# Kernel tuning notes

Measured on AMD Instinct MI355X. Metric: run time of the kernel, lower is better.

The kernel has to match this reference:

```python
import jax, jax.numpy as jnp
import numpy as np

IMAGE_SIZE = 192
NEAR = 0.1
FAR = 100.0
EPS = 1e-3
BACKGROUND = (0.0, 0.0, 0.0)


def setup_inputs() -> dict:
    key = jax.random.key(0)
    k1, k2, k3, k4 = jax.random.split(key, 4)
    B, F, T = 2, 512, 4
    centers = jax.random.uniform(k1, (B, F, 1, 2), minval=-0.9, maxval=0.9)
    offsets = jax.random.normal(k2, (B, F, 3, 2)) * 0.08
    xy = centers + offsets  # triangle vertices in NDC [-1, 1]
    z = jax.random.uniform(k3, (B, F, 3, 1), minval=1.0, maxval=10.0)  # inside (near, far)
    faces = jnp.concatenate([xy, z], axis=-1).astype(jnp.float32)  # [B,F,3,3]
    textures = jax.random.uniform(k4, (B, F, T, T, T, 3), dtype=jnp.float32)
    return {"faces": faces, "textures": textures}


def _face_inv(v):
    # v: [..., 3 verts, 3 (x,y,z)]. Rows of cofactor matrix / det give barycentric coeffs
    # so that w_k = row_k . (px, py, 1), matching rasterize_cuda's face_inv.
    x0, y0 = v[..., 0, 0], v[..., 0, 1]
    x1, y1 = v[..., 1, 0], v[..., 1, 1]
    x2, y2 = v[..., 2, 0], v[..., 2, 1]
    det = x2 * (y0 - y1) + x0 * (y1 - y2) + x1 * (y2 - y0)
    det = jnp.where(jnp.abs(det) < 1e-12, 1e-12, det)
    rows = jnp.stack([
        y1 - y2, x2 - x1, x1 * y2 - x2 * y1,
        y2 - y0, x0 - x2, x2 * y0 - x0 * y2,
        y0 - y1, x1 - x0, x0 * y1 - x1 * y0], axis=-1)
    return rows.reshape(v.shape[:-2] + (3, 3)) / det[..., None, None]


def _rasterize(faces, textures):
    B, F = faces.shape[:2]
    T = textures.shape[2]
    IS = IMAGE_SIZE
    P = IS * IS
    # pixel centers in NDC, matching (2*i + 1 - is) / is in the CUDA kernel
    coord = (2.0 * jnp.arange(IS, dtype=faces.dtype) + 1.0 - IS) / IS
    yp, xp = jnp.meshgrid(coord, coord, indexing="ij")
    xp = xp.reshape(P)
    yp = yp.reshape(P)
    pc = jnp.stack([xp, yp, jnp.ones((P,), faces.dtype)], axis=-1)  # [P,3]

    x = faces[..., 0]
    y = faces[..., 1]
    z = faces[..., 2]  # [B,F,3]
    # backface culling (skip if (y2-y0)*(x1-x0) < (y1-y0)*(x2-x0))
    front = (y[..., 2] - y[..., 0]) * (x[..., 1] - x[..., 0]) >= \
            (x[..., 2] - x[..., 0]) * (y[..., 1] - y[..., 0])  # [B,F]

    def edge_ok(a, b):
        # pixel on inner side of edge a->b: (yp-ya)*(xb-xa) >= (xp-xa)*(yb-ya)
        return ((yp[None, None, :] - y[..., a:a + 1]) * (x[..., b:b + 1] - x[..., a:a + 1])
                >= (xp[None, None, :] - x[..., a:a + 1]) * (y[..., b:b + 1] - y[..., a:a + 1]))

    inside = edge_ok(0, 1) & edge_ok(1, 2) & edge_ok(2, 0)  # [B,F,P]

    finv = _face_inv(faces)  # [B,F,3,3]
    w = jnp.einsum("bfkc,pc->bfpk", finv, pc)  # barycentric weights [B,F,P,3]
    w = jnp.clip(w, 0.0, 1.0)
    w = w / jnp.maximum(jnp.sum(w, axis=-1, keepdims=True), 1e-12)
    # perspective-correct depth: 1/zp = sum_k w_k / z_k
    zp = 1.0 / jnp.maximum(jnp.einsum("bfpk,bfk->bfp", w, 1.0 / z), 1e-12)
    valid = front[..., None] & inside & (zp > NEAR) & (zp < FAR)
    depth_c = jnp.where(valid, zp, FAR)
    depth_map = jnp.min(depth_c, axis=1)  # z-buffer [B,P]
    fidx = jnp.argmin(depth_c, axis=1)    # winning face per pixel (ties -> lowest index)
    found = depth_map < FAR

    # gather barycentric weights / vertices of the winning face
    wwin = jnp.take_along_axis(w, fidx[:, None, :, None], axis=1)[:, 0]  # [B,P,3]
    vwin = jax.vmap(lambda f, i: f[i])(faces, fidx)  # [B,P,3,3]
    zwin = vwin[..., 2]  # [B,P,3]

    # texture-cube trilinear sampling with perspective-corrected weights
    tif = wwin * (T - 1) * (depth_map[..., None] / zwin)
    tif = jnp.clip(tif, 0.0, T - 1 - EPS)
    tlo_f = jnp.floor(tif)
    frac = tif - tlo_f
    tlo = tlo_f.astype(jnp.int32)
    bits = (jnp.arange(8)[:, None] >> jnp.arange(3)[None, :]) & 1  # [8,3] corner offsets
    idx = tlo[..., None, :] + bits  # [B,P,8,3], in [0, T-1]
    cw = jnp.prod(jnp.where(bits.astype(bool), frac[..., None, :], 1.0 - frac[..., None, :]), axis=-1)  # [B,P,8]
    fsafe = jnp.maximum(fidx, 0)
    flat = ((fsafe[..., None] * T + idx[..., 0]) * T + idx[..., 1]) * T + idx[..., 2]  # [B,P,8]
    texf = textures.reshape(B, F * T * T * T, 3)
    samp = jax.vmap(lambda t, i: t[i])(texf, flat)  # [B,P,8,3]
    rgb = jnp.sum(cw[..., None] * samp, axis=-2)  # [B,P,3]
    bg = jnp.asarray(BACKGROUND, dtype=rgb.dtype)
    rgb = jnp.where(found[..., None], rgb, bg)  # background compositing

    rgb_map = rgb.reshape(B, IS, IS, 3)
    alpha_map = found.astype(faces.dtype).reshape(B, 1, IS, IS)  # single part (part_mask=None)
    depth_out = depth_map.reshape(B, IS, IS)
    return rgb_map, alpha_map, depth_out


def reference(faces, textures):
    return _rasterize(faces, textures)
```

## Files before the change

kernel.cpp:

```cpp
#include <hip/hip_runtime.h>

#define IS     192
#define F_CNT  512
#define TEX    4
#define NEARF  0.1f
#define FARF   100.0f

struct FaceData {
    float xmin, xmax, ymin, ymax;
    float x0, y0, x1, y1, x2, y2;
    float f00, f01, f02, f10, f11, f12, f20, f21, f22;
    float iz0, iz1, iz2;
    float z0, z1, z2;
};

__global__ __launch_bounds__(256) void raster_kernel(
    const float* __restrict__ faces,
    const float* __restrict__ textures,
    float* __restrict__ out)
{
    __shared__ FaceData sf[F_CNT];
    __shared__ unsigned short sidx[F_CNT];
    __shared__ int scount;

    const int b   = blockIdx.z;
    const int tx0 = blockIdx.x * 16;
    const int ty0 = blockIdx.y * 16;
    const int tid = threadIdx.y * 16 + threadIdx.x;

    if (tid == 0) scount = 0;
    __syncthreads();

    const float xlo = (2.0f * tx0        + 1.0f - IS) / (float)IS;
    const float xhi = (2.0f * (tx0 + 15) + 1.0f - IS) / (float)IS;
    const float ylo = (2.0f * ty0        + 1.0f - IS) / (float)IS;
    const float yhi = (2.0f * (ty0 + 15) + 1.0f - IS) / (float)IS;

    for (int f = tid; f < F_CNT; f += 256) {
        const float* v = faces + ((size_t)b * F_CNT + f) * 9;
        const float x0 = v[0], y0 = v[1], z0 = v[2];
        const float x1 = v[3], y1 = v[4], z1 = v[5];
        const float x2 = v[6], y2 = v[7], z2 = v[8];

        const bool front = (y2 - y0) * (x1 - x0) >= (x2 - x0) * (y1 - y0);

        const float bxmin = fminf(x0, fminf(x1, x2));
        const float bxmax = fmaxf(x0, fmaxf(x1, x2));
        const float bymin = fminf(y0, fminf(y1, y2));
        const float bymax = fmaxf(y0, fmaxf(y1, y2));

        const bool keep = front &&
                          bxmin <= xhi && bxmax >= xlo &&
                          bymin <= yhi && bymax >= ylo;
        if (keep) {
            FaceData fd;
            fd.xmin = bxmin; fd.xmax = bxmax; fd.ymin = bymin; fd.ymax = bymax;
            fd.x0 = x0; fd.y0 = y0; fd.x1 = x1; fd.y1 = y1; fd.x2 = x2; fd.y2 = y2;

            float det = x2 * (y0 - y1) + x0 * (y1 - y2) + x1 * (y2 - y0);
            if (fabsf(det) < 1e-12f) det = 1e-12f;
            fd.f00 = (y1 - y2) / det;
            fd.f01 = (x2 - x1) / det;
            fd.f02 = (x1 * y2 - x2 * y1) / det;
            fd.f10 = (y2 - y0) / det;
            fd.f11 = (x0 - x2) / det;
            fd.f12 = (x2 * y0 - x0 * y2) / det;
            fd.f20 = (y0 - y1) / det;
            fd.f21 = (x1 - x0) / det;
            fd.f22 = (x0 * y1 - x1 * y0) / det;

            fd.iz0 = 1.0f / z0; fd.iz1 = 1.0f / z1; fd.iz2 = 1.0f / z2;
            fd.z0 = z0; fd.z1 = z1; fd.z2 = z2;

            sf[f] = fd;
            const int slot = atomicAdd(&scount, 1);
            sidx[slot] = (unsigned short)f;
        }
    }
    __syncthreads();

    const int px = tx0 + threadIdx.x;
    const int py = ty0 + threadIdx.y;
    const float xp = (2.0f * px + 1.0f - IS) / (float)IS;
    const float yp = (2.0f * py + 1.0f - IS) / (float)IS;

    float best = FARF;
    int bestf = -1;
    float bw0 = 0.0f, bw1 = 0.0f, bw2 = 0.0f;

    const int cnt = scount;
    for (int i = 0; i < cnt; ++i) {
        const int f = sidx[i];
        const FaceData& fd = sf[f];

        if (xp < fd.xmin || xp > fd.xmax || yp < fd.ymin || yp > fd.ymax) continue;

        const bool in01 = (yp - fd.y0) * (fd.x1 - fd.x0) >= (xp - fd.x0) * (fd.y1 - fd.y0);
        const bool in12 = (yp - fd.y1) * (fd.x2 - fd.x1) >= (xp - fd.x1) * (fd.y2 - fd.y1);
        const bool in20 = (yp - fd.y2) * (fd.x0 - fd.x2) >= (xp - fd.x2) * (fd.y0 - fd.y2);
        if (!(in01 && in12 && in20)) continue;

        float w0 = fd.f00 * xp + fd.f01 * yp + fd.f02;
        float w1 = fd.f10 * xp + fd.f11 * yp + fd.f12;
        float w2 = fd.f20 * xp + fd.f21 * yp + fd.f22;
        w0 = fminf(fmaxf(w0, 0.0f), 1.0f);
        w1 = fminf(fmaxf(w1, 0.0f), 1.0f);
        w2 = fminf(fmaxf(w2, 0.0f), 1.0f);
        const float ws = fmaxf(w0 + w1 + w2, 1e-12f);
        w0 = w0 / ws; w1 = w1 / ws; w2 = w2 / ws;

        const float s = w0 * fd.iz0 + w1 * fd.iz1 + w2 * fd.iz2;
        const float zp = 1.0f / fmaxf(s, 1e-12f);

        if (zp > NEARF && zp < FARF) {
            if (zp < best || (zp == best && f < bestf)) {
                best = zp; bestf = f;
                bw0 = w0; bw1 = w1; bw2 = w2;
            }
        }
    }

    float r = 0.0f, g = 0.0f, bc = 0.0f;
    if (bestf >= 0) {
        const FaceData& fd = sf[bestf];
        float t0 = bw0 * 3.0f * (best / fd.z0);
        float t1 = bw1 * 3.0f * (best / fd.z1);
        float t2 = bw2 * 3.0f * (best / fd.z2);
        const float tmax = 2.999f;
        t0 = fminf(fmaxf(t0, 0.0f), tmax);
        t1 = fminf(fmaxf(t1, 0.0f), tmax);
        t2 = fminf(fmaxf(t2, 0.0f), tmax);
        const float fl0 = floorf(t0), fl1 = floorf(t1), fl2 = floorf(t2);
        const float fr0 = t0 - fl0, fr1 = t1 - fl1, fr2 = t2 - fl2;
        const int i0 = (int)fl0, i1 = (int)fl1, i2 = (int)fl2;

        const float* tex = textures + ((size_t)b * F_CNT + bestf) * (TEX * TEX * TEX * 3);
        #pragma unroll
        for (int c = 0; c < 8; ++c) {
            const int b0 = c & 1, b1 = (c >> 1) & 1, b2 = (c >> 2) & 1;
            const float cw = (b0 ? fr0 : 1.0f - fr0)
                           * (b1 ? fr1 : 1.0f - fr1)
                           * (b2 ? fr2 : 1.0f - fr2);
            const float* sp = tex + (((size_t)(i0 + b0) * TEX + (i1 + b1)) * TEX + (i2 + b2)) * 3;
            r  += cw * sp[0];
            g  += cw * sp[1];
            bc += cw * sp[2];
        }
    }

    const size_t pix = (size_t)py * IS + px;
    const size_t bp  = (size_t)b * IS * IS + pix;

    out[bp * 3 + 0] = r;
    out[bp * 3 + 1] = g;
    out[bp * 3 + 2] = bc;

    float* alpha = out + (size_t)2 * IS * IS * 3;
    alpha[bp] = (bestf >= 0) ? 1.0f : 0.0f;

    float* depth = alpha + (size_t)2 * IS * IS;
    depth[bp] = best;
}

extern "C" void kernel_launch(void* const* d_in, const int* in_sizes, int n_in,
                              void* d_out, int out_size, void* d_ws, size_t ws_size,
                              hipStream_t stream) {
    const float* faces    = (const float*)d_in[0];
    const float* textures = (const float*)d_in[1];
    float* out = (float*)d_out;

    const int B = in_sizes[0] / (F_CNT * 9);

    dim3 grid(IS / 16, IS / 16, B);
    dim3 block(16, 16, 1);
    raster_kernel<<<grid, block, 0, stream>>>(faces, textures, out);
}
```

Measured before the change: 14.85 us.

## Shrink tiles to 8x8 and compact culled faces into capped shared buffer

Pixel tiles shrink from 16x16 to 8x8 with one 64-thread wavefront per block, giving 4x more blocks and tighter per-tile face culling. Face setup data is now stored compactly in slot order in a 256-entry shared array sized by capacity, so the raster loop reads shared memory contiguously. Faces past the capacity are rebuilt from global memory on the fly. Per-face setup moves after the cull test, and the winning face's z values are kept in registers for texturing. The cost is that each face's culling and setup is repeated across four times as many blocks.

New measurement: 16.28 us. 9.7% more time.

```diff
diff --git a/kernel.cpp b/kernel.cpp
--- a/kernel.cpp
+++ b/kernel.cpp
@@ -5,42 +5,74 @@
 #define TEX    4
 #define NEARF  0.1f
 #define FARF   100.0f
+#define TSZ    8
+#define CAP    256
 
-struct FaceData {
+struct alignas(16) FaceData {
     float xmin, xmax, ymin, ymax;
     float x0, y0, x1, y1, x2, y2;
     float f00, f01, f02, f10, f11, f12, f20, f21, f22;
     float iz0, iz1, iz2;
     float z0, z1, z2;
+    float pad0, pad1, pad2;
 };
 
-__global__ __launch_bounds__(256) void raster_kernel(
+__device__ inline FaceData make_face(const float* __restrict__ v) {
+    FaceData fd;
+    const float x0 = v[0], y0 = v[1], z0 = v[2];
+    const float x1 = v[3], y1 = v[4], z1 = v[5];
+    const float x2 = v[6], y2 = v[7], z2 = v[8];
+
+    fd.xmin = fminf(x0, fminf(x1, x2));
+    fd.xmax = fmaxf(x0, fmaxf(x1, x2));
+    fd.ymin = fminf(y0, fminf(y1, y2));
+    fd.ymax = fmaxf(y0, fmaxf(y1, y2));
+    fd.x0 = x0; fd.y0 = y0; fd.x1 = x1; fd.y1 = y1; fd.x2 = x2; fd.y2 = y2;
+
+    float det = x2 * (y0 - y1) + x0 * (y1 - y2) + x1 * (y2 - y0);
+    if (fabsf(det) < 1e-12f) det = 1e-12f;
+    fd.f00 = (y1 - y2) / det;
+    fd.f01 = (x2 - x1) / det;
+    fd.f02 = (x1 * y2 - x2 * y1) / det;
+    fd.f10 = (y2 - y0) / det;
+    fd.f11 = (x0 - x2) / det;
+    fd.f12 = (x2 * y0 - x0 * y2) / det;
+    fd.f20 = (y0 - y1) / det;
+    fd.f21 = (x1 - x0) / det;
+    fd.f22 = (x0 * y1 - x1 * y0) / det;
+
+    fd.iz0 = 1.0f / z0; fd.iz1 = 1.0f / z1; fd.iz2 = 1.0f / z2;
+    fd.z0 = z0; fd.z1 = z1; fd.z2 = z2;
+    return fd;
+}
+
+__global__ __launch_bounds__(64) void raster_kernel(
     const float* __restrict__ faces,
     const float* __restrict__ textures,
     float* __restrict__ out)
 {
-    __shared__ FaceData sf[F_CNT];
+    __shared__ FaceData sf[CAP];
     __shared__ unsigned short sidx[F_CNT];
     __shared__ int scount;
 
     const int b   = blockIdx.z;
-    const int tx0 = blockIdx.x * 16;
-    const int ty0 = blockIdx.y * 16;
-    const int tid = threadIdx.y * 16 + threadIdx.x;
+    const int tx0 = blockIdx.x * TSZ;
+    const int ty0 = blockIdx.y * TSZ;
+    const int tid = threadIdx.y * TSZ + threadIdx.x;
 
     if (tid == 0) scount = 0;
     __syncthreads();
 
-    const float xlo = (2.0f * tx0        + 1.0f - IS) / (float)IS;
-    const float xhi = (2.0f * (tx0 + 15) + 1.0f - IS) / (float)IS;
-    const float ylo = (2.0f * ty0        + 1.0f - IS) / (float)IS;
-    const float yhi = (2.0f * (ty0 + 15) + 1.0f - IS) / (float)IS;
+    const float xlo = (2.0f * tx0             + 1.0f - IS) / (float)IS;
+    const float xhi = (2.0f * (tx0 + TSZ - 1) + 1.0f - IS) / (float)IS;
+    const float ylo = (2.0f * ty0             + 1.0f - IS) / (float)IS;
+    const float yhi = (2.0f * (ty0 + TSZ - 1) + 1.0f - IS) / (float)IS;
 
-    for (int f = tid; f < F_CNT; f += 256) {
+    for (int f = tid; f < F_CNT; f += 64) {
         const float* v = faces + ((size_t)b * F_CNT + f) * 9;
-        const float x0 = v[0], y0 = v[1], z0 = v[2];
-        const float x1 = v[3], y1 = v[4], z1 = v[5];
-        const float x2 = v[6], y2 = v[7], z2 = v[8];
+        const float x0 = v[0], y0 = v[1];
+        const float x1 = v[3], y1 = v[4];
+        const float x2 = v[6], y2 = v[7];
 
         const bool front = (y2 - y0) * (x1 - x0) >= (x2 - x0) * (y1 - y0);
 
@@ -53,28 +85,9 @@
                           bxmin <= xhi && bxmax >= xlo &&
                           bymin <= yhi && bymax >= ylo;
         if (keep) {
-            FaceData fd;
-            fd.xmin = bxmin; fd.xmax = bxmax; fd.ymin = bymin; fd.ymax = bymax;
-            fd.x0 = x0; fd.y0 = y0; fd.x1 = x1; fd.y1 = y1; fd.x2 = x2; fd.y2 = y2;
-
-            float det = x2 * (y0 - y1) + x0 * (y1 - y2) + x1 * (y2 - y0);
-            if (fabsf(det) < 1e-12f) det = 1e-12f;
-            fd.f00 = (y1 - y2) / det;
-            fd.f01 = (x2 - x1) / det;
-            fd.f02 = (x1 * y2 - x2 * y1) / det;
-            fd.f10 = (y2 - y0) / det;
-            fd.f11 = (x0 - x2) / det;
-            fd.f12 = (x2 * y0 - x0 * y2) / det;
-            fd.f20 = (y0 - y1) / det;
-            fd.f21 = (x1 - x0) / det;
-            fd.f22 = (x0 * y1 - x1 * y0) / det;
-
-            fd.iz0 = 1.0f / z0; fd.iz1 = 1.0f / z1; fd.iz2 = 1.0f / z2;
-            fd.z0 = z0; fd.z1 = z1; fd.z2 = z2;
-
-            sf[f] = fd;
             const int slot = atomicAdd(&scount, 1);
             sidx[slot] = (unsigned short)f;
+            if (slot < CAP) sf[slot] = make_face(v);
         }
     }
     __syncthreads();
@@ -87,18 +100,15 @@
     float best = FARF;
     int bestf = -1;
     float bw0 = 0.0f, bw1 = 0.0f, bw2 = 0.0f;
+    float bz0 = 1.0f, bz1 = 1.0f, bz2 = 1.0f;
 
-    const int cnt = scount;
-    for (int i = 0; i < cnt; ++i) {
-        const int f = sidx[i];
-        const FaceData& fd = sf[f];
-
-        if (xp < fd.xmin || xp > fd.xmax || yp < fd.ymin || yp > fd.ymax) continue;
+    auto process = [&](const FaceData& fd, const int f) {
+        if (xp < fd.xmin || xp > fd.xmax || yp < fd.ymin || yp > fd.ymax) return;
 
         const bool in01 = (yp - fd.y0) * (fd.x1 - fd.x0) >= (xp - fd.x0) * (fd.y1 - fd.y0);
         const bool in12 = (yp - fd.y1) * (fd.x2 - fd.x1) >= (xp - fd.x1) * (fd.y2 - fd.y1);
         const bool in20 = (yp - fd.y2) * (fd.x0 - fd.x2) >= (xp - fd.x2) * (fd.y0 - fd.y2);
-        if (!(in01 && in12 && in20)) continue;
+        if (!(in01 && in12 && in20)) return;
 
         float w0 = fd.f00 * xp + fd.f01 * yp + fd.f02;
         float w1 = fd.f10 * xp + fd.f11 * yp + fd.f12;
@@ -116,16 +126,26 @@
             if (zp < best || (zp == best && f < bestf)) {
                 best = zp; bestf = f;
                 bw0 = w0; bw1 = w1; bw2 = w2;
+                bz0 = fd.z0; bz1 = fd.z1; bz2 = fd.z2;
             }
         }
+    };
+
+    const int cnt = scount;
+    const int ncached = (cnt < CAP) ? cnt : CAP;
+    for (int i = 0; i < ncached; ++i)
+        process(sf[i], sidx[i]);
+    for (int i = CAP; i < cnt; ++i) {
+        const int f = sidx[i];
+        const FaceData fd = make_face(faces + ((size_t)b * F_CNT + f) * 9);
+        process(fd, f);
     }
 
     float r = 0.0f, g = 0.0f, bc = 0.0f;
     if (bestf >= 0) {
-        const FaceData& fd = sf[bestf];
-        float t0 = bw0 * 3.0f * (best / fd.z0);
-        float t1 = bw1 * 3.0f * (best / fd.z1);
-        float t2 = bw2 * 3.0f * (best / fd.z2);
+        float t0 = bw0 * 3.0f * (best / bz0);
+        float t1 = bw1 * 3.0f * (best / bz1);
+        float t2 = bw2 * 3.0f * (best / bz2);
         const float tmax = 2.999f;
         t0 = fminf(fmaxf(t0, 0.0f), tmax);
         t1 = fminf(fmaxf(t1, 0.0f), tmax);
@@ -171,7 +191,7 @@
 
     const int B = in_sizes[0] / (F_CNT * 9);
 
-    dim3 grid(IS / 16, IS / 16, B);
-    dim3 block(16, 16, 1);
+    dim3 grid(IS / TSZ, IS / TSZ, B);
+    dim3 block(TSZ, TSZ, 1);
     raster_kernel<<<grid, block, 0, stream>>>(faces, textures, out);
 }
```
